# Performance work log

Hardware: AMD Instinct MI355X
Metric: run time of the kernel (lower is better)

## Reference

```python
import jax, jax.numpy as jnp
import numpy as np

N_NODES = 50000
N_EDGES = 500000
NEG_SLOPE = 0.2


def gat_layer(x, src, dst, W, a_src, a_dst, b, n):
    """PyG-style GATConv (add_self_loops=True, concat=True, eval mode).
    x: [N, F_in], W: [F_in, H*C], a_src/a_dst: [H, C], b: [H*C]."""
    H, C = a_src.shape
    h = (x @ W).reshape(-1, H, C)              # [N, H, C]
    loops = jnp.arange(n, dtype=src.dtype)
    s = jnp.concatenate([src, loops])          # self-loops appended
    d = jnp.concatenate([dst, loops])
    alpha_src = jnp.einsum('nhc,hc->nh', h, a_src)   # [N, H]
    alpha_dst = jnp.einsum('nhc,hc->nh', h, a_dst)
    e = jax.nn.leaky_relu(alpha_src[s] + alpha_dst[d], NEG_SLOPE)  # [E+N, H]
    m = jax.ops.segment_max(e, d, num_segments=n)    # segment softmax over dst
    w = jnp.exp(e - m[d])
    denom = jax.ops.segment_sum(w, d, num_segments=n)
    attn = w / (denom[d] + 1e-16)                    # [E+N, H]
    msg = h[s] * attn[:, :, None]                    # [E+N, H, C]
    out = jax.ops.segment_sum(msg, d, num_segments=n)  # [N, H, C]
    return out.reshape(n, H * C) + b


def setup_inputs() -> dict:
    key = jax.random.key(0)
    ks = jax.random.split(key, 20)
    F_in, Hd, Hh = 128, 64, 4
    g = lambda k, shp, fan: jax.random.normal(k, shp, jnp.float32) * (1.0 / np.sqrt(fan))
    inp = {
        'x': jax.random.normal(ks[0], (N_NODES, F_in), jnp.float32),
        'edge_index': jax.random.randint(ks[1], (2, N_EDGES), 0, N_NODES, jnp.int32),
        'W1': g(ks[2], (F_in, Hh * Hd), F_in),
        'a1s': g(ks[3], (Hh, Hd), Hd), 'a1d': g(ks[4], (Hh, Hd), Hd),
        'b1': jnp.zeros((Hh * Hd,), jnp.float32),
        'W2': g(ks[5], (Hh * Hd, Hh * Hd), Hh * Hd),
        'a2s': g(ks[6], (Hh, Hd), Hd), 'a2d': g(ks[7], (Hh, Hd), Hd),
        'b2': jnp.zeros((Hh * Hd,), jnp.float32),
        'W3': g(ks[8], (Hh * Hd, Hd), Hh * Hd),
        'a3s': g(ks[9], (1, Hd), Hd), 'a3d': g(ks[10], (1, Hd), Hd),
        'b3': jnp.zeros((Hd,), jnp.float32),
        'cW1': g(ks[11], (Hd, Hd // 2), Hd), 'cb1': jnp.zeros((Hd // 2,), jnp.float32),
        'cW2': g(ks[12], (Hd // 2, 2), Hd // 2), 'cb2': jnp.zeros((2,), jnp.float32),
    }
    return inp


def reference(x, edge_index, W1, a1s, a1d, b1, W2, a2s, a2d, b2,
              W3, a3s, a3d, b3, cW1, cb1, cW2, cb2):
    n = x.shape[0]
    src, dst = edge_index[0], edge_index[1]
    h = jax.nn.elu(gat_layer(x, src, dst, W1, a1s, a1d, b1, n))
    h = jax.nn.elu(gat_layer(h, src, dst, W2, a2s, a2d, b2, n))
    h = jax.nn.relu(gat_layer(h, src, dst, W3, a3s, a3d, b3, n))
    h = jax.nn.relu(h @ cW1 + cb1)
    logits = h @ cW2 + cb2
    return jax.nn.log_softmax(logits, axis=1)
```

## Files before the change

kernel.cpp:

```cpp
#include <hip/hip_runtime.h>
#include <hip/hip_fp16.h>

#define LRELU(v) ((v) > 0.f ? (v) : 0.2f * (v))
#define LOG2E 1.44269504088896340736f

typedef _Float16 f16x8 __attribute__((ext_vector_type(8)));
typedef _Float16 f16x2 __attribute__((ext_vector_type(2)));
typedef float f32x4 __attribute__((ext_vector_type(4)));

__device__ __forceinline__ float fexp2(float x) {
    return __builtin_amdgcn_exp2f(x);
}

__global__ __launch_bounds__(256) void hist_kernel(const int* __restrict__ dst,
                                                   int* __restrict__ cnt, int E) {
    int e = blockIdx.x * 256 + threadIdx.x;
    if (e < E) atomicAdd(&cnt[dst[e]], 1);
}

__global__ __launch_bounds__(256) void scan_blk(const int* __restrict__ cnt,
                                                int* __restrict__ offv,
                                                int* __restrict__ bsum, int N) {
    __shared__ int sh[256];
    const int t = threadIdx.x;
    const int base = blockIdx.x * 1024 + t * 4;
    int v0 = (base + 0 < N) ? cnt[base + 0] : 0;
    int v1 = (base + 1 < N) ? cnt[base + 1] : 0;
    int v2 = (base + 2 < N) ? cnt[base + 2] : 0;
    int v3 = (base + 3 < N) ? cnt[base + 3] : 0;
    const int T = v0 + v1 + v2 + v3;
    sh[t] = T;
    __syncthreads();
    for (int o = 1; o < 256; o <<= 1) {
        int x = (t >= o) ? sh[t - o] : 0;
        __syncthreads();
        sh[t] += x;
        __syncthreads();
    }
    const int excl = sh[t] - T;
    if (t == 255) bsum[blockIdx.x] = sh[255];
    if (base + 0 < N) offv[base + 0] = excl;
    if (base + 1 < N) offv[base + 1] = excl + v0;
    if (base + 2 < N) offv[base + 2] = excl + v0 + v1;
    if (base + 3 < N) offv[base + 3] = excl + v0 + v1 + v2;
}

__global__ __launch_bounds__(64) void scan_top(int* __restrict__ bsum,
                                               int* __restrict__ offv,
                                               int NB, int N) {
    const int t = threadIdx.x;
    const int v = (t < NB) ? bsum[t] : 0;
    int incl = v;
#pragma unroll
    for (int o = 1; o < 64; o <<= 1) {
        int x = __shfl_up(incl, o);
        if (t >= o) incl += x;
    }
    if (t < NB) bsum[t] = incl - v;
    if (t == NB - 1) offv[N] = incl;
}

__global__ __launch_bounds__(256) void scan_add(int* __restrict__ offv,
                                                const int* __restrict__ bsum, int N) {
    const int base = blockIdx.x * 1024 + threadIdx.x * 4;
    const int add = bsum[blockIdx.x];
#pragma unroll
    for (int i = 0; i < 4; ++i)
        if (base + i < N) offv[base + i] += add;
}

__global__ __launch_bounds__(256) void fill_kernel(const int* __restrict__ dst,
                                                   const int* __restrict__ srcv,
                                                   const int* __restrict__ offv,
                                                   int* __restrict__ cnt,
                                                   int* __restrict__ csrsrc, int E) {
    int e = blockIdx.x * 256 + threadIdx.x;
    if (e < E) {
        int d = dst[e];
        int p = atomicSub(&cnt[d], 1);
        csrsrc[offv[d] + p - 1] = srcv[e];
    }
}

__global__ __launch_bounds__(256) void prep_w_all(
    const float* __restrict__ W1, const float* __restrict__ W2,
    const float* __restrict__ W3, _Float16* __restrict__ Wt1,
    _Float16* __restrict__ Wt2, _Float16* __restrict__ Wt3) {
    const int S1 = 128 * 256, S2 = 256 * 256, S3 = 256 * 64;
    int idx = blockIdx.x * 256 + threadIdx.x;
    if (idx < S1) {
        int k = idx >> 8, nn = idx & 255;
        Wt1[nn * 128 + k] = (_Float16)W1[idx];
    } else if (idx < S1 + S2) {
        int i = idx - S1;
        int k = i >> 8, nn = i & 255;
        Wt2[nn * 256 + k] = (_Float16)W2[i];
    } else if (idx < S1 + S2 + S3) {
        int i = idx - S1 - S2;
        int k = i >> 6, nn = i & 63;
        Wt3[nn * 256 + k] = (_Float16)W3[i];
    }
}

template <int K, bool AF32>
__global__ __launch_bounds__(256) void gemm64_fused(
    const void* __restrict__ Av, const _Float16* __restrict__ Wt,
    const float* __restrict__ a_s, const float* __restrict__ a_d,
    _Float16* __restrict__ hout, float* __restrict__ als,
    float* __restrict__ ald, int M) {
    constexpr int NKC = K / 64;
    __shared__ f16x8 Atile[2][512];
    const _Float16* A16 = (const _Float16*)Av;
    const float* A32 = (const float*)Av;
    const int t = threadIdx.x;
    const int lane = t & 63;
    const int wn = t >> 6;
    const int m0 = blockIdx.x * 64;
    const int l15 = lane & 15, lg = lane >> 4;

    const int r0 = t >> 3, c0 = t & 7;
    const int r1 = (t + 256) >> 3, c1 = t & 7;
    const int gr0 = min(m0 + r0, M - 1);
    const int gr1 = min(m0 + r1, M - 1);

    f16x8 s0, s1;
    auto FETCH = [&](int kc) {
        if constexpr (AF32) {
            float4 p = *(const float4*)(A32 + (size_t)gr0 * K + kc + c0 * 8);
            float4 q = *(const float4*)(A32 + (size_t)gr0 * K + kc + c0 * 8 + 4);
            s0[0] = (_Float16)p.x; s0[1] = (_Float16)p.y;
            s0[2] = (_Float16)p.z; s0[3] = (_Float16)p.w;
            s0[4] = (_Float16)q.x; s0[5] = (_Float16)q.y;
            s0[6] = (_Float16)q.z; s0[7] = (_Float16)q.w;
            float4 r = *(const float4*)(A32 + (size_t)gr1 * K + kc + c1 * 8);
            float4 u = *(const float4*)(A32 + (size_t)gr1 * K + kc + c1 * 8 + 4);
            s1[0] = (_Float16)r.x; s1[1] = (_Float16)r.y;
            s1[2] = (_Float16)r.z; s1[3] = (_Float16)r.w;
            s1[4] = (_Float16)u.x; s1[5] = (_Float16)u.y;
            s1[6] = (_Float16)u.z; s1[7] = (_Float16)u.w;
        } else {
            s0 = *(const f16x8*)(A16 + (size_t)gr0 * K + kc + c0 * 8);
            s1 = *(const f16x8*)(A16 + (size_t)gr1 * K + kc + c1 * 8);
        }
    };
    FETCH(0);

    f32x4 acc[4][4];
    const f32x4 zz = {0.f, 0.f, 0.f, 0.f};
#pragma unroll
    for (int mi = 0; mi < 4; ++mi)
#pragma unroll
        for (int ni = 0; ni < 4; ++ni) acc[mi][ni] = zz;

    int cur = 0;
#pragma unroll
    for (int kci = 0; kci < NKC; ++kci) {
        Atile[cur][r0 * 8 + (c0 ^ (r0 & 7))] = s0;
        Atile[cur][r1 * 8 + (c1 ^ (r1 & 7))] = s1;
        __syncthreads();
        if (kci + 1 < NKC) FETCH((kci + 1) * 64);
#pragma unroll
        for (int ks = 0; ks < 2; ++ks) {
            f16x8 af[4], bf[4];
#pragma unroll
            for (int mi = 0; mi < 4; ++mi) {
                const int row = mi * 16 + l15;
                af[mi] = Atile[cur][row * 8 + ((ks * 4 + lg) ^ (row & 7))];
            }
#pragma unroll
            for (int ni = 0; ni < 4; ++ni) {
                const int col = wn * 64 + ni * 16 + l15;
                bf[ni] = *(const f16x8*)(Wt + (size_t)col * K + kci * 64 + ks * 32 + lg * 8);
            }
#pragma unroll
            for (int mi = 0; mi < 4; ++mi)
#pragma unroll
                for (int ni = 0; ni < 4; ++ni)
                    acc[mi][ni] = __builtin_amdgcn_mfma_f32_16x16x32_f16(
                        af[mi], bf[ni], acc[mi][ni], 0, 0, 0);
        }
        cur ^= 1;
    }
    const int head = wn;
    float a4s[4], a4d[4];
#pragma unroll
    for (int ni = 0; ni < 4; ++ni) {
        a4s[ni] = a_s[head * 64 + ni * 16 + l15] * LOG2E;
        a4d[ni] = a_d[head * 64 + ni * 16 + l15] * LOG2E;
    }
#pragma unroll
    for (int mi = 0; mi < 4; ++mi)
#pragma unroll
        for (int j = 0; j < 4; ++j) {
            const int r = m0 + mi * 16 + lg * 4 + j;
            if (r < M) {
                float s1v = 0.f, s2v = 0.f;
#pragma unroll
                for (int ni = 0; ni < 4; ++ni) {
                    const float v = acc[mi][ni][j];
                    s1v += v * a4s[ni];
                    s2v += v * a4d[ni];
                    hout[(size_t)r * 256 + wn * 64 + ni * 16 + l15] = (_Float16)v;
                }
#pragma unroll
                for (int o = 8; o; o >>= 1) {
                    s1v += __shfl_xor(s1v, o);
                    s2v += __shfl_xor(s2v, o);
                }
                if (l15 == 0) {
                    als[(size_t)r * 4 + head] = s1v;
                    ald[(size_t)r * 4 + head] = s2v;
                }
            }
        }
}

template <int K>
__global__ __launch_bounds__(256) void gemm64n64_fused(
    const _Float16* __restrict__ A16, const _Float16* __restrict__ Wt,
    const float* __restrict__ a_s, const float* __restrict__ a_d,
    _Float16* __restrict__ hout, float* __restrict__ als,
    float* __restrict__ ald, int M) {
    constexpr int NKC = K / 64;
    __shared__ f16x8 Atile[2][512];
    const int t = threadIdx.x;
    const int lane = t & 63;
    const int wv = t >> 6;
    const int m0 = blockIdx.x * 64;
    const int l15 = lane & 15, lg = lane >> 4;

    const int r0 = t >> 3, c0 = t & 7;
    const int r1 = (t + 256) >> 3, c1 = t & 7;
    const int gr0 = min(m0 + r0, M - 1);
    const int gr1 = min(m0 + r1, M - 1);

    f16x8 s0, s1;
    auto FETCH = [&](int kc) {
        s0 = *(const f16x8*)(A16 + (size_t)gr0 * K + kc + c0 * 8);
        s1 = *(const f16x8*)(A16 + (size_t)gr1 * K + kc + c1 * 8);
    };
    FETCH(0);

    f32x4 acc[4];
    const f32x4 zz = {0.f, 0.f, 0.f, 0.f};
#pragma unroll
    for (int ni = 0; ni < 4; ++ni) acc[ni] = zz;

    int cur = 0;
#pragma unroll
    for (int kci = 0; kci < NKC; ++kci) {
        Atile[cur][r0 * 8 + (c0 ^ (r0 & 7))] = s0;
        Atile[cur][r1 * 8 + (c1 ^ (r1 & 7))] = s1;
        __syncthreads();
        if (kci + 1 < NKC) FETCH((kci + 1) * 64);
#pragma unroll
        for (int ks = 0; ks < 2; ++ks) {
            const int row = wv * 16 + l15;
            const f16x8 af = Atile[cur][row * 8 + ((ks * 4 + lg) ^ (row & 7))];
            f16x8 bf[4];
#pragma unroll
            for (int ni = 0; ni < 4; ++ni) {
                const int col = ni * 16 + l15;
                bf[ni] = *(const f16x8*)(Wt + (size_t)col * K + kci * 64 + ks * 32 + lg * 8);
            }
#pragma unroll
            for (int ni = 0; ni < 4; ++ni)
                acc[ni] = __builtin_amdgcn_mfma_f32_16x16x32_f16(
                    af, bf[ni], acc[ni], 0, 0, 0);
        }
        cur ^= 1;
    }
    float a4s[4], a4d[4];
#pragma unroll
    for (int ni = 0; ni < 4; ++ni) {
        a4s[ni] = a_s[ni * 16 + l15] * LOG2E;
        a4d[ni] = a_d[ni * 16 + l15] * LOG2E;
    }
#pragma unroll
    for (int j = 0; j < 4; ++j) {
        const int r = m0 + wv * 16 + lg * 4 + j;
        if (r < M) {
            float s1v = 0.f, s2v = 0.f;
#pragma unroll
            for (int ni = 0; ni < 4; ++ni) {
                const float v = acc[ni][j];
                s1v += v * a4s[ni];
                s2v += v * a4d[ni];
                hout[(size_t)r * 64 + ni * 16 + l15] = (_Float16)v;
            }
#pragma unroll
            for (int o = 8; o; o >>= 1) {
                s1v += __shfl_xor(s1v, o);
                s2v += __shfl_xor(s2v, o);
            }
            if (l15 == 0) {
                als[r] = s1v;
                ald[r] = s2v;
            }
        }
    }
}

__global__ __launch_bounds__(256) void gat_agg_h4(
    const _Float16* __restrict__ hhf, const float4* __restrict__ als4,
    const float4* __restrict__ ald4, const int* __restrict__ csrsrc,
    const int* __restrict__ offv, const float* __restrict__ bias,
    _Float16* __restrict__ outh, int N) {
    __shared__ int sidAll[4][2][36];
    __shared__ float wTAll[4][2][4][36];
    const int wv = threadIdx.x >> 6;
    const int l = threadIdx.x & 63;
    const int half = l >> 5;
    const int q = l & 31;
    const int n = (blockIdx.x * 4 + wv) * 2 + half;
    if (n >= N) return;
    const int hh = q >> 3;
    int* sid = sidAll[wv][half];
    float* wrow = wTAll[wv][half][hh];
    float (*wT)[36] = wTAll[wv][half];
    const int start = offv[n];
    const int deg = offv[n + 1] - start;
    const float4 ad = ald4[n];
    const float4 asf = als4[n];
    float4 ws4;
    ws4.x = fexp2(LRELU(asf.x + ad.x));
    ws4.y = fexp2(LRELU(asf.y + ad.y));
    ws4.z = fexp2(LRELU(asf.z + ad.z));
    ws4.w = fexp2(LRELU(asf.w + ad.w));
    float wself = ws4.x;
    wself = (hh == 1) ? ws4.y : wself;
    wself = (hh == 2) ? ws4.z : wself;
    wself = (hh == 3) ? ws4.w : wself;
    float accA[8], accB[8] = {};
    {
        const f16x8 hv = *(const f16x8*)(hhf + (size_t)n * 256 + q * 8);
#pragma unroll
        for (int c = 0; c < 8; ++c) accA[c] = (float)hv[c] * wself;
    }
    float dsum = wself;

    for (int base = 0; base < deg; base += 32) {
        const int nb = min(32, deg - base);
        int s = 0;
        float4 w4 = {0.f, 0.f, 0.f, 0.f};
        if (q < nb) {
            s = csrsrc[start + base + q];
            const float4 av = als4[s];
            w4.x = fexp2(LRELU(av.x + ad.x));
            w4.y = fexp2(LRELU(av.y + ad.y));
            w4.z = fexp2(LRELU(av.z + ad.z));
            w4.w = fexp2(LRELU(av.w + ad.w));
        }
        sid[q] = s;
        wT[0][q] = w4.x;
        wT[1][q] = w4.y;
        wT[2][q] = w4.z;
        wT[3][q] = w4.w;
        __threadfence_block();
        int i = 0;
        for (; i + 1 < nb; i += 2) {
            const int sA = sid[i], sB = sid[i + 1];
            const float wA = wrow[i], wB = wrow[i + 1];
            const f16x8 hA = *(const f16x8*)(hhf + (size_t)sA * 256 + q * 8);
            const f16x8 hB = *(const f16x8*)(hhf + (size_t)sB * 256 + q * 8);
            dsum += wA + wB;
#pragma unroll
            for (int c = 0; c < 8; ++c) {
                accA[c] += (float)hA[c] * wA;
                accB[c] += (float)hB[c] * wB;
            }
        }
        if (i < nb) {
            const int sA = sid[i];
            const float wA = wrow[i];
            const f16x8 hA = *(const f16x8*)(hhf + (size_t)sA * 256 + q * 8);
            dsum += wA;
#pragma unroll
            for (int c = 0; c < 8; ++c) accA[c] += (float)hA[c] * wA;
        }
        __threadfence_block();
    }
    const float inv = 1.f / (dsum + 1e-16f);
    const float4 bv0 = *(const float4*)(bias + q * 8);
    const float4 bv1 = *(const float4*)(bias + q * 8 + 4);
    float o8[8];
#pragma unroll
    for (int c = 0; c < 8; ++c) o8[c] = (accA[c] + accB[c]) * inv;
    o8[0] += bv0.x; o8[1] += bv0.y; o8[2] += bv0.z; o8[3] += bv0.w;
    o8[4] += bv1.x; o8[5] += bv1.y; o8[6] += bv1.z; o8[7] += bv1.w;
#pragma unroll
    for (int c = 0; c < 8; ++c)
        o8[c] = (o8[c] > 0.f) ? o8[c] : (__expf(o8[c]) - 1.f);
    f16x8 st;
#pragma unroll
    for (int c = 0; c < 8; ++c) st[c] = (_Float16)o8[c];
    *(f16x8*)(outh + (size_t)n * 256 + q * 8) = st;
}

__global__ __launch_bounds__(256) void gat_agg_h1(
    const _Float16* __restrict__ hhf, const float* __restrict__ als,
    const float* __restrict__ ald, const int* __restrict__ csrsrc,
    const int* __restrict__ offv, const float* __restrict__ bias,
    _Float16* __restrict__ outh, int N) {
    __shared__ int sidAll[4][2][36];
    __shared__ float wAll[4][2][36];
    const int wv = threadIdx.x >> 6;
    const int l = threadIdx.x & 63;
    const int half = l >> 5;
    const int q = l & 31;
    const int n = (blockIdx.x * 4 + wv) * 2 + half;
    if (n >= N) return;
    int* sid = sidAll[wv][half];
    float* wsh = wAll[wv][half];
    const int start = offv[n];
    const int deg = offv[n + 1] - start;
    const float ad = ald[n];
    const float wself = fexp2(LRELU(als[n] + ad));
    float acc0, acc1;
    {
        const f16x2 hv = *(const f16x2*)(hhf + (size_t)n * 64 + q * 2);
        acc0 = (float)hv[0] * wself;
        acc1 = (float)hv[1] * wself;
    }
    float dsum = wself;

    for (int base = 0; base < deg; base += 32) {
        const int nb = min(32, deg - base);
        int s = 0;
        float w = 0.f;
        if (q < nb) {
            s = csrsrc[start + base + q];
            w = fexp2(LRELU(als[s] + ad));
        }
        sid[q] = s;
        wsh[q] = w;
        __threadfence_block();
        for (int i = 0; i < nb; ++i) {
            const int si = sid[i];
            const float wi = wsh[i];
            const f16x2 hv = *(const f16x2*)(hhf + (size_t)si * 64 + q * 2);
            dsum += wi;
            acc0 += (float)hv[0] * wi;
            acc1 += (float)hv[1] * wi;
        }
        __threadfence_block();
    }
    const float inv = 1.f / (dsum + 1e-16f);
    const float v0 = fmaxf(acc0 * inv + bias[q * 2], 0.f);
    const float v1 = fmaxf(acc1 * inv + bias[q * 2 + 1], 0.f);
    f16x2 st;
    st[0] = (_Float16)v0;
    st[1] = (_Float16)v1;
    *(f16x2*)(outh + (size_t)n * 64 + q * 2) = st;
}

__global__ __launch_bounds__(256) void classifier_ls(
    const _Float16* __restrict__ h3, const float* __restrict__ cW1,
    const float* __restrict__ cb1, const float* __restrict__ cW2,
    const float* __restrict__ cb2, float* __restrict__ outp, int N) {
    __shared__ float w1s[2048];
    __shared__ float w2s[64];
    __shared__ float b1s[32];
    for (int i = threadIdx.x; i < 2048; i += 256) w1s[i] = cW1[i];
    if (threadIdx.x < 64) w2s[threadIdx.x] = cW2[threadIdx.x];
    if (threadIdx.x < 32) b1s[threadIdx.x] = cb1[threadIdx.x];
    __syncthreads();
    const int n = blockIdx.x * 256 + threadIdx.x;
    if (n >= N) return;
    float x[64];
#pragma unroll
    for (int i = 0; i < 8; ++i) {
        const f16x8 v = *(const f16x8*)(h3 + (size_t)n * 64 + i * 8);
#pragma unroll
        for (int j = 0; j < 8; ++j) x[i * 8 + j] = (float)v[j];
    }
    float l0 = cb2[0], l1 = cb2[1];
    for (int j = 0; j < 32; ++j) {
        float s = b1s[j];
#pragma unroll
        for (int c = 0; c < 64; ++c) s += x[c] * w1s[c * 32 + j];
        s = fmaxf(s, 0.f);
        l0 += s * w2s[j * 2];
        l1 += s * w2s[j * 2 + 1];
    }
    const float mm = fmaxf(l0, l1);
    const float lse = mm + logf(__expf(l0 - mm) + __expf(l1 - mm));
    outp[(size_t)n * 2 + 0] = l0 - lse;
    outp[(size_t)n * 2 + 1] = l1 - lse;
}

extern "C" void kernel_launch(void* const* d_in, const int* in_sizes, int n_in,
                              void* d_out, int out_size, void* d_ws, size_t ws_size,
                              hipStream_t stream) {
    const float* x   = (const float*)d_in[0];
    const int*   ei  = (const int*)d_in[1];
    const float* W1  = (const float*)d_in[2];
    const float* a1s = (const float*)d_in[3];
    const float* a1d = (const float*)d_in[4];
    const float* b1  = (const float*)d_in[5];
    const float* W2  = (const float*)d_in[6];
    const float* a2s = (const float*)d_in[7];
    const float* a2d = (const float*)d_in[8];
    const float* b2  = (const float*)d_in[9];
    const float* W3  = (const float*)d_in[10];
    const float* a3s = (const float*)d_in[11];
    const float* a3d = (const float*)d_in[12];
    const float* b3  = (const float*)d_in[13];
    const float* cW1 = (const float*)d_in[14];
    const float* cb1 = (const float*)d_in[15];
    const float* cW2 = (const float*)d_in[16];
    const float* cb2 = (const float*)d_in[17];

    const int N = in_sizes[0] / 128;
    const int E = in_sizes[1] / 2;
    const int* srcv = ei;
    const int* dstv = ei + E;

    char* p = (char*)d_ws;
    _Float16* slotA = (_Float16*)p; p += (size_t)N * 256 * 2;
    _Float16* slotB = (_Float16*)p; p += (size_t)N * 256 * 2;
    float* als = (float*)p; p += (size_t)N * 4 * 4;
    float* ald = (float*)p; p += (size_t)N * 4 * 4;
    int* cnt = (int*)p; p += (size_t)N * 4;
    int* offv = (int*)p; p += (size_t)(N + 4) * 4;
    int* csr = (int*)p; p += (size_t)E * 4;
    _Float16* Wt1 = (_Float16*)p; p += (size_t)128 * 256 * 2;
    _Float16* Wt2 = (_Float16*)p; p += (size_t)256 * 256 * 2;
    _Float16* Wt3 = (_Float16*)p; p += (size_t)256 * 64 * 2;
    int* bsum = (int*)p;

    prep_w_all<<<(128 * 256 + 256 * 256 + 256 * 64 + 255) / 256, 256, 0, stream>>>(
        W1, W2, W3, Wt1, Wt2, Wt3);

    const int NB = (N + 1023) / 1024;
    hipMemsetAsync(cnt, 0, (size_t)N * sizeof(int), stream);
    hist_kernel<<<(E + 255) / 256, 256, 0, stream>>>(dstv, cnt, E);
    scan_blk<<<NB, 256, 0, stream>>>(cnt, offv, bsum, N);
    scan_top<<<1, 64, 0, stream>>>(bsum, offv, NB, N);
    scan_add<<<NB, 256, 0, stream>>>(offv, bsum, N);
    fill_kernel<<<(E + 255) / 256, 256, 0, stream>>>(dstv, srcv, offv, cnt, csr, E);

    const int MB64 = (N + 63) / 64;
    const int AGG8 = (N + 7) / 8;
    const int CLS = (N + 255) / 256;

    gemm64_fused<128, true><<<MB64, 256, 0, stream>>>(
        x, Wt1, a1s, a1d, slotA, als, ald, N);
    gat_agg_h4<<<AGG8, 256, 0, stream>>>(slotA, (const float4*)als,
                                         (const float4*)ald, csr, offv, b1,
                                         slotB, N);

    gemm64_fused<256, false><<<MB64, 256, 0, stream>>>(
        slotB, Wt2, a2s, a2d, slotA, als, ald, N);
    gat_agg_h4<<<AGG8, 256, 0, stream>>>(slotA, (const float4*)als,
                                         (const float4*)ald, csr, offv, b2,
                                         slotB, N);

    gemm64n64_fused<256><<<MB64, 256, 0, stream>>>(
        slotB, Wt3, a3s, a3d, slotA, als, ald, N);
    gat_agg_h1<<<AGG8, 256, 0, stream>>>(slotA, als, ald, csr, offv, b3,
                                         slotB, N);

    classifier_ls<<<CLS, 256, 0, stream>>>(slotB, cW1, cb1, cW2, cb2,
                                           (float*)d_out, N);
}
```

Before: 274.6 us.

## Fuse classifier into last GAT aggregation and merge scan top/add kernels

The final single-head GAT aggregation now runs the two-layer classifier and log-softmax in the same kernel. Each 32-lane half-wave stages its node's 64 features in shared memory, computes one hidden unit per lane, and reduces the logits with shuffles, which avoids writing and re-reading h3 and saves a launch. The scan_top and scan_add kernels are also merged, with every block computing its own prefix from the block sums by a wave reduction. In exchange, every aggregation block now loads the 8KB classifier weights into shared memory and adds a barrier. The higher LDS use may lower occupancy.

```diff
diff --git a/kernel.cpp b/kernel.cpp
--- a/kernel.cpp
+++ b/kernel.cpp
@@ -45,25 +45,29 @@
     if (base + 3 < N) offv[base + 3] = excl + v0 + v1 + v2;
 }
 
-__global__ __launch_bounds__(64) void scan_top(int* __restrict__ bsum,
-                                               int* __restrict__ offv,
-                                               int NB, int N) {
+__global__ __launch_bounds__(256) void scan_add2(int* __restrict__ offv,
+                                                 const int* __restrict__ bsum,
+                                                 int NB, int N) {
+    __shared__ int s_add;
     const int t = threadIdx.x;
-    const int v = (t < NB) ? bsum[t] : 0;
-    int incl = v;
-#pragma unroll
-    for (int o = 1; o < 64; o <<= 1) {
-        int x = __shfl_up(incl, o);
-        if (t >= o) incl += x;
-    }
-    if (t < NB) bsum[t] = incl - v;
-    if (t == NB - 1) offv[N] = incl;
-}
-
-__global__ __launch_bounds__(256) void scan_add(int* __restrict__ offv,
-                                                const int* __restrict__ bsum, int N) {
-    const int base = blockIdx.x * 1024 + threadIdx.x * 4;
-    const int add = bsum[blockIdx.x];
+    const int b = blockIdx.x;
+    if (t < 64) {
+        int v = (t < NB) ? bsum[t] : 0;
+        int pre = (t < b) ? v : 0;
+        int tot = v;
+#pragma unroll
+        for (int o = 32; o; o >>= 1) {
+            pre += __shfl_xor(pre, o);
+            tot += __shfl_xor(tot, o);
+        }
+        if (t == 0) {
+            s_add = pre;
+            if (b == NB - 1) offv[N] = tot;
+        }
+    }
+    __syncthreads();
+    const int add = s_add;
+    const int base = b * 1024 + t * 4;
 #pragma unroll
     for (int i = 0; i < 4; ++i)
         if (base + i < N) offv[base + i] += add;
@@ -397,13 +401,23 @@
     *(f16x8*)(outh + (size_t)n * 256 + q * 8) = st;
 }
 
-__global__ __launch_bounds__(256) void gat_agg_h1(
+__global__ __launch_bounds__(256) void gat_agg_h1_cls(
     const _Float16* __restrict__ hhf, const float* __restrict__ als,
     const float* __restrict__ ald, const int* __restrict__ csrsrc,
     const int* __restrict__ offv, const float* __restrict__ bias,
-    _Float16* __restrict__ outh, int N) {
+    const float* __restrict__ cW1, const float* __restrict__ cb1,
+    const float* __restrict__ cW2, const float* __restrict__ cb2,
+    float* __restrict__ outp, int N) {
+    __shared__ float w1s[2048];
+    __shared__ float w2s[64];
+    __shared__ float b1s[32];
     __shared__ int sidAll[4][2][36];
     __shared__ float wAll[4][2][36];
+    __shared__ float xsAll[4][2][64];
+    for (int i = threadIdx.x; i < 2048; i += 256) w1s[i] = cW1[i];
+    if (threadIdx.x < 64) w2s[threadIdx.x] = cW2[threadIdx.x];
+    if (threadIdx.x < 32) b1s[threadIdx.x] = cb1[threadIdx.x];
+    __syncthreads();
     const int wv = threadIdx.x >> 6;
     const int l = threadIdx.x & 63;
     const int half = l >> 5;
@@ -412,6 +426,7 @@
     if (n >= N) return;
     int* sid = sidAll[wv][half];
     float* wsh = wAll[wv][half];
+    float* xs = xsAll[wv][half];
     const int start = offv[n];
     const int deg = offv[n + 1] - start;
     const float ad = ald[n];
@@ -448,45 +463,28 @@
     const float inv = 1.f / (dsum + 1e-16f);
     const float v0 = fmaxf(acc0 * inv + bias[q * 2], 0.f);
     const float v1 = fmaxf(acc1 * inv + bias[q * 2 + 1], 0.f);
-    f16x2 st;
-    st[0] = (_Float16)v0;
-    st[1] = (_Float16)v1;
-    *(f16x2*)(outh + (size_t)n * 64 + q * 2) = st;
-}
-
-__global__ __launch_bounds__(256) void classifier_ls(
-    const _Float16* __restrict__ h3, const float* __restrict__ cW1,
-    const float* __restrict__ cb1, const float* __restrict__ cW2,
-    const float* __restrict__ cb2, float* __restrict__ outp, int N) {
-    __shared__ float w1s[2048];
-    __shared__ float w2s[64];
-    __shared__ float b1s[32];
-    for (int i = threadIdx.x; i < 2048; i += 256) w1s[i] = cW1[i];
-    if (threadIdx.x < 64) w2s[threadIdx.x] = cW2[threadIdx.x];
-    if (threadIdx.x < 32) b1s[threadIdx.x] = cb1[threadIdx.x];
-    __syncthreads();
-    const int n = blockIdx.x * 256 + threadIdx.x;
-    if (n >= N) return;
-    float x[64];
-#pragma unroll
-    for (int i = 0; i < 8; ++i) {
-        const f16x8 v = *(const f16x8*)(h3 + (size_t)n * 64 + i * 8);
-#pragma unroll
-        for (int j = 0; j < 8; ++j) x[i * 8 + j] = (float)v[j];
-    }
-    float l0 = cb2[0], l1 = cb2[1];
-    for (int j = 0; j < 32; ++j) {
-        float s = b1s[j];
-#pragma unroll
-        for (int c = 0; c < 64; ++c) s += x[c] * w1s[c * 32 + j];
-        s = fmaxf(s, 0.f);
-        l0 += s * w2s[j * 2];
-        l1 += s * w2s[j * 2 + 1];
-    }
+    xs[q * 2] = v0;
+    xs[q * 2 + 1] = v1;
+    __threadfence_block();
+    float s1 = b1s[q];
+#pragma unroll 8
+    for (int c = 0; c < 64; ++c) s1 += xs[c] * w1s[c * 32 + q];
+    const float hid = fmaxf(s1, 0.f);
+    float c0 = hid * w2s[q * 2];
+    float c1 = hid * w2s[q * 2 + 1];
+#pragma unroll
+    for (int o = 16; o; o >>= 1) {
+        c0 += __shfl_xor(c0, o);
+        c1 += __shfl_xor(c1, o);
+    }
+    const float l0 = c0 + cb2[0];
+    const float l1 = c1 + cb2[1];
     const float mm = fmaxf(l0, l1);
     const float lse = mm + logf(__expf(l0 - mm) + __expf(l1 - mm));
-    outp[(size_t)n * 2 + 0] = l0 - lse;
-    outp[(size_t)n * 2 + 1] = l1 - lse;
+    if (q == 0) {
+        outp[(size_t)n * 2 + 0] = l0 - lse;
+        outp[(size_t)n * 2 + 1] = l1 - lse;
+    }
 }
 
 extern "C" void kernel_launch(void* const* d_in, const int* in_sizes, int n_in,
@@ -536,13 +534,11 @@
     hipMemsetAsync(cnt, 0, (size_t)N * sizeof(int), stream);
     hist_kernel<<<(E + 255) / 256, 256, 0, stream>>>(dstv, cnt, E);
     scan_blk<<<NB, 256, 0, stream>>>(cnt, offv, bsum, N);
-    scan_top<<<1, 64, 0, stream>>>(bsum, offv, NB, N);
-    scan_add<<<NB, 256, 0, stream>>>(offv, bsum, N);
+    scan_add2<<<NB, 256, 0, stream>>>(offv, bsum, NB, N);
     fill_kernel<<<(E + 255) / 256, 256, 0, stream>>>(dstv, srcv, offv, cnt, csr, E);
 
     const int MB64 = (N + 63) / 64;
     const int AGG8 = (N + 7) / 8;
-    const int CLS = (N + 255) / 256;
 
     gemm64_fused<128, true><<<MB64, 256, 0, stream>>>(
         x, Wt1, a1s, a1d, slotA, als, ald, N);
@@ -558,9 +554,7 @@
 
     gemm64n64_fused<256><<<MB64, 256, 0, stream>>>(
         slotB, Wt3, a3s, a3d, slotA, als, ald, N);
-    gat_agg_h1<<<AGG8, 256, 0, stream>>>(slotA, als, ald, csr, offv, b3,
-                                         slotB, N);
-
-    classifier_ls<<<CLS, 256, 0, stream>>>(slotB, cW1, cb1, cW2, cb2,
-                                           (float*)d_out, N);
-}
+    gat_agg_h1_cls<<<AGG8, 256, 0, stream>>>(slotA, als, ald, csr, offv, b3,
+                                             cW1, cb1, cW2, cb2,
+                                             (float*)d_out, N);
+}
```

New measurement: 257.7 us. 1.07x faster.
